# Optimization experiments

Measured on AMD Instinct MI355X. Metric: run time of the kernel, lower is better.

## Reference

```python
import jax, jax.numpy as jnp
import numpy as np


def setup_inputs() -> dict:
    key = jax.random.key(0)
    k1, k2 = jax.random.split(key)
    B, D, H, W, K = 16, 256, 32, 32, 8192
    x = jax.random.normal(k1, (B, D, H, W), dtype=jnp.float32)
    # init_tensor: uniform [0,1), L2-normalized along dim 0 (embedding_dim), * embedding_scale
    e = jax.random.uniform(k2, (D, K), dtype=jnp.float32)
    e_i_ts = e / jnp.linalg.norm(e, axis=0, keepdims=True)
    return {"x": x, "e_i_ts": e_i_ts}


def reference(x, e_i_ts):
    B, D = x.shape[0], x.shape[1]
    spatial = x.shape[2:]
    # permute [B, D, *spatial] -> [B, *spatial, D], flatten tokens
    perm = (0,) + tuple(range(2, x.ndim)) + (1,)
    flat_x = jnp.transpose(x, perm).reshape(-1, D)  # [N, D]
    distances = (
        jnp.sum(flat_x * flat_x, axis=1, keepdims=True)
        - 2.0 * (flat_x @ e_i_ts)
        + jnp.sum(e_i_ts * e_i_ts, axis=0, keepdims=True)
    )
    encoding_indices = jnp.argmin(distances, axis=1)  # [N]
    ind = encoding_indices.reshape((B,) + spatial)  # [B, *spatial]
    # gather codebook columns: e_i_ts.T[ind] -> [B, *spatial, D], back to channel-first
    quantized = jnp.take(e_i_ts.T, ind, axis=0)
    inv_perm = (0, x.ndim - 1) + tuple(range(1, x.ndim - 1))
    quantized_x = jnp.transpose(quantized, inv_perm)  # [B, D, *spatial]
    # straight-through estimator
    quantized_x_d = x + jax.lax.stop_gradient(quantized_x - x)
    return quantized_x_d, quantized_x, ind
```

## Files before the change

### kernel.cpp

```cpp
#include <hip/hip_runtime.h>
#include <hip/hip_bf16.h>
#include <hip/hip_fp16.h>


#define D_   256
#define HW_  1024
#define N_   16384
#define K_   8192
#define NB_  32
#define MARGIN 0.02f

#define OUT1_OFF 4194304
#define IND_OFF  8388608

typedef __attribute__((ext_vector_type(8))) _Float16 f16x8;
typedef __attribute__((ext_vector_type(4))) float f32x4;

__device__ __forceinline__ unsigned long long pack_dk(float dist, int k) {
    unsigned db = __float_as_uint(dist);
    unsigned mono = (db & 0x80000000u) ? ~db : (db | 0x80000000u);
    return ((unsigned long long)mono << 32) | (unsigned)k;
}

__device__ __forceinline__ void async_copy16(const void* g, void* l) {
    __builtin_amdgcn_global_load_lds(
        (const __attribute__((address_space(1))) void*)g,
        (__attribute__((address_space(3))) void*)l, 16, 0, 0);
}

__global__ __launch_bounds__(256)
void cnorm_kernel(const float* __restrict__ E, float* __restrict__ c,
                  int* __restrict__ counters) {
    if (blockIdx.x == 0 && threadIdx.x < 2) counters[threadIdx.x] = 0;
    __shared__ float part[8][32];
    const int tid = threadIdx.x;
    const int cl = tid & 31, q = tid >> 5;
    const int k = blockIdx.x * 32 + cl;
    float s = 0.f;
    #pragma unroll 8
    for (int d = q * 32; d < q * 32 + 32; ++d) {
        float v = E[(size_t)d * K_ + k];
        s = fmaf(v, v, s);
    }
    part[q][cl] = s;
    __syncthreads();
    if (tid < 32) {
        float t0 = (part[0][tid] + part[1][tid]) + (part[2][tid] + part[3][tid]);
        float t1 = (part[4][tid] + part[5][tid]) + (part[6][tid] + part[7][tid]);
        c[blockIdx.x * 32 + tid] = t0 + t1;
    }
}

__global__ __launch_bounds__(256)
void prep_x(const float* __restrict__ x, ushort* __restrict__ xf) {
    __shared__ float t[32][33];
    const int s0 = blockIdx.x * 32, d0 = blockIdx.y * 32, b = blockIdx.z;
    const int tid = threadIdx.x;
    #pragma unroll
    for (int j = 0; j < 4; ++j) {
        int i = tid + 256 * j; int dd = i >> 5, ss = i & 31;
        t[dd][ss] = x[(size_t)b * 262144 + (size_t)(d0 + dd) * 1024 + s0 + ss];
    }
    __syncthreads();
    #pragma unroll
    for (int j = 0; j < 4; ++j) {
        int i = tid + 256 * j; int ss = i >> 5, dd = i & 31;
        _Float16 h = (_Float16)t[dd][ss];
        size_t o = (size_t)(b * 1024 + s0 + ss) * D_ + d0 + dd;
        xf[o] = *(ushort*)&h;
    }
}

__global__ __launch_bounds__(256)
void prep_e(const float* __restrict__ E, ushort* __restrict__ ef) {
    __shared__ float t[32][33];
    const int k0 = blockIdx.x * 32, d0 = blockIdx.y * 32;
    const int tid = threadIdx.x;
    #pragma unroll
    for (int j = 0; j < 4; ++j) {
        int i = tid + 256 * j; int dd = i >> 5, kk = i & 31;
        t[dd][kk] = E[(size_t)(d0 + dd) * K_ + k0 + kk];
    }
    __syncthreads();
    #pragma unroll
    for (int j = 0; j < 4; ++j) {
        int i = tid + 256 * j; int kk = i >> 5, dd = i & 31;
        _Float16 h = (_Float16)t[dd][kk];
        ef[(size_t)(k0 + kk) * D_ + d0 + dd] = *(ushort*)&h;
    }
}

__global__ __launch_bounds__(256, 3)
void mfma_kernel(const ushort* __restrict__ xf,
                 const ushort* __restrict__ ef,
                 const float* __restrict__ c,
                 float* __restrict__ pd1, int* __restrict__ pi1, float* __restrict__ pd2) {
    __shared__ __align__(16) ushort Ah[2][2048];
    __shared__ __align__(16) ushort Bb[2][8192];
    __shared__ float redm1[320], redm2[320];
    __shared__ int   redi1[320];

    const int tid = threadIdx.x;
    const int bid = blockIdx.x;
    const int xcd = bid & 7, rr = bid >> 3;
    const int nb = rr >> 5, mb = xcd * 32 + (rr & 31);
    const int n0 = mb * 64, k0 = nb * 256;
    const int lane = tid & 63, w = tid >> 6;
    const int l15 = lane & 15, lq = lane >> 4;

    size_t aoff;
    {
        int slot = w * 64 + lane;
        int t = slot >> 2, cp = slot & 3;
        int cs = cp ^ ((t >> 1) & 3);
        aoff = (size_t)(n0 + t) * D_ + cs * 8;
    }
    const int adst = w * 512;
    size_t boff[4]; int bdst[4];
    #pragma unroll
    for (int g = 0; g < 4; ++g) {
        int slot = (w * 4 + g) * 64 + lane;
        int t = slot >> 2, cp = slot & 3;
        int cs = cp ^ ((t >> 1) & 3);
        boff[g] = (size_t)(k0 + t) * D_ + cs * 8;
        bdst[g] = (w * 4 + g) * 512;
    }
    int aro[4], bro[4];
    #pragma unroll
    for (int mt = 0; mt < 4; ++mt) {
        int R = mt * 16 + l15;
        aro[mt] = R * 32 + ((lq ^ ((R >> 1) & 3)) * 8);
    }
    #pragma unroll
    for (int nt = 0; nt < 4; ++nt) {
        int R = w * 64 + nt * 16 + l15;
        bro[nt] = R * 32 + ((lq ^ ((R >> 1) & 3)) * 8);
    }

    f32x4 acc[4][4];
    #pragma unroll
    for (int mt = 0; mt < 4; ++mt)
        #pragma unroll
        for (int nt = 0; nt < 4; ++nt) acc[mt][nt] = (f32x4){0.f, 0.f, 0.f, 0.f};

    async_copy16(xf + aoff, &Ah[0][adst]);
    #pragma unroll
    for (int g = 0; g < 4; ++g)
        async_copy16(ef + boff[g], &Bb[0][bdst[g]]);
    __syncthreads();

    #pragma unroll
    for (int db = 0; db < 8; ++db) {
        const int cur = db & 1;
        const int d0 = db * 32;
        if (db < 7) {
            const int dn = d0 + 32;
            async_copy16(xf + aoff + dn, &Ah[cur ^ 1][adst]);
            #pragma unroll
            for (int g = 0; g < 4; ++g)
                async_copy16(ef + boff[g] + dn, &Bb[cur ^ 1][bdst[g]]);
        }
        f16x8 a[4], b[4];
        #pragma unroll
        for (int mt = 0; mt < 4; ++mt)
            a[mt] = *(const f16x8*)&Ah[cur][aro[mt]];
        #pragma unroll
        for (int nt = 0; nt < 4; ++nt)
            b[nt] = *(const f16x8*)&Bb[cur][bro[nt]];
        #pragma unroll
        for (int nt = 0; nt < 4; ++nt)
            #pragma unroll
            for (int mt = 0; mt < 4; ++mt)
                acc[mt][nt] = __builtin_amdgcn_mfma_f32_16x16x32_f16(a[mt], b[nt], acc[mt][nt], 0, 0, 0);
        __syncthreads();
    }

    float cv[4];
    #pragma unroll
    for (int nt = 0; nt < 4; ++nt) cv[nt] = c[k0 + w * 64 + nt * 16 + l15];

    float m1[16], m2[16]; int i1[16];
    #pragma unroll
    for (int mt = 0; mt < 4; ++mt)
        #pragma unroll
        for (int r = 0; r < 4; ++r) {
            int p = mt * 4 + r;
            float a = 3.4e38f, b2 = 3.4e38f; int ai = -1;
            #pragma unroll
            for (int nt = 0; nt < 4; ++nt) {
                float d = fmaf(-2.f, acc[mt][nt][r], cv[nt]);
                int k = k0 + w * 64 + nt * 16 + l15;
                if (d < a) { b2 = a; a = d; ai = k; } else if (d < b2) b2 = d;
            }
            m1[p] = a; i1[p] = ai; m2[p] = b2;
        }
    #pragma unroll
    for (int s = 1; s < 16; s <<= 1) {
        #pragma unroll
        for (int p = 0; p < 16; ++p) {
            float n1 = __shfl_xor(m1[p], s);
            int   ni = __shfl_xor(i1[p], s);
            float n2 = __shfl_xor(m2[p], s);
            if (n1 < m1[p]) { m2[p] = fminf(m1[p], n2); m1[p] = n1; i1[p] = ni; }
            else            { m2[p] = fminf(m2[p], n1); }
        }
    }
    if (l15 == 0) {
        #pragma unroll
        for (int mt = 0; mt < 4; ++mt)
            #pragma unroll
            for (int r = 0; r < 4; ++r) {
                int p = mt * 4 + r;
                int t = mt * 16 + lq * 4 + r;
                redm1[t * 5 + w] = m1[p]; redi1[t * 5 + w] = i1[p]; redm2[t * 5 + w] = m2[p];
            }
    }
    __syncthreads();
    if (tid < 64) {
        float a = redm1[tid * 5], b2 = redm2[tid * 5]; int ai = redi1[tid * 5];
        #pragma unroll
        for (int q = 1; q < 4; ++q) {
            float n1 = redm1[tid * 5 + q], n2 = redm2[tid * 5 + q]; int ni = redi1[tid * 5 + q];
            if (n1 < a) { b2 = fminf(a, n2); a = n1; ai = ni; }
            else        { b2 = fminf(b2, n1); }
        }
        size_t o = (size_t)nb * N_ + n0 + tid;
        pd1[o] = a; pi1[o] = ai; pd2[o] = b2;
    }
}

__global__ __launch_bounds__(256)
void merge_flag(const float* __restrict__ pd1, const int* __restrict__ pi1,
                const float* __restrict__ pd2,
                int* __restrict__ idx, int* __restrict__ counters,
                unsigned long long* __restrict__ key,
                unsigned int* __restrict__ pairs, unsigned int* __restrict__ scans) {
    int n = blockIdx.x * 256 + threadIdx.x;
    float a = 3.4e38f, b2 = 3.4e38f; int ai = -1;
    for (int nb = 0; nb < NB_; ++nb) {
        float n1 = pd1[(size_t)nb * N_ + n];
        int   ni = pi1[(size_t)nb * N_ + n];
        float n2 = pd2[(size_t)nb * N_ + n];
        if (n1 < a) { b2 = fminf(a, n2); a = n1; ai = ni; }
        else        { b2 = fminf(b2, n1); }
    }
    if (b2 - a < MARGIN) {
        const float W = a + MARGIN;
        key[n] = ~0ULL;
        idx[n] = 0x80000000 | ai;
        for (int nb = 0; nb < NB_; ++nb) {
            if (pd2[(size_t)nb * N_ + n] <= W) {
                int q = atomicAdd(&counters[1], 1);
                scans[q] = ((unsigned)n << 5) | (unsigned)nb;
            } else if (pd1[(size_t)nb * N_ + n] <= W) {
                int q = atomicAdd(&counters[0], 1);
                pairs[q] = ((unsigned)n << 13) | (unsigned)pi1[(size_t)nb * N_ + n];
            }
        }
    } else {
        idx[n] = ai;
    }
}

__global__ __launch_bounds__(256)
void recheck(const float* __restrict__ x, const float* __restrict__ E,
             const float* __restrict__ c, const unsigned int* __restrict__ pairs,
             const unsigned int* __restrict__ scans, const int* __restrict__ counters,
             unsigned long long* __restrict__ key) {
    if (blockIdx.x < 128) {
        int items = counters[0] * 4;
        for (int it = blockIdx.x * 256 + threadIdx.x; it < items; it += 128 * 256) {
            int p = it >> 2, q = it & 3;
            unsigned v = pairs[p];
            int n = v >> 13, k = v & 8191;
            int b = n >> 10, s = n & 1023;
            const float* xb = x + (size_t)b * 262144 + s;
            const float* eb = E + k;
            float acc = 0.f;
            const int d0 = q * 64;
            #pragma unroll 8
            for (int d = d0; d < d0 + 64; ++d)
                acc = fmaf(xb[(size_t)d * HW_], eb[(size_t)d * K_], acc);
            float o1 = __shfl_xor(acc, 1); float s2 = acc + o1;
            float o2 = __shfl_xor(s2, 2);  float tot = s2 + o2;
            if (q == 0) atomicMin(key + n, pack_dk(fmaf(-2.f, tot, c[k]), k));
        }
    } else {
        int cnt = counters[1];
        for (int t = blockIdx.x - 128; t < cnt; t += 256) {
            unsigned v = scans[t];
            int n = v >> 5, nb = v & 31;
            int k = nb * 256 + threadIdx.x;
            int b = n >> 10, s = n & 1023;
            const float* xb = x + (size_t)b * 262144 + s;
            float acc = 0.f;
            #pragma unroll 4
            for (int d = 0; d < D_; ++d)
                acc = fmaf(xb[(size_t)d * HW_], E[(size_t)d * K_ + k], acc);
            float dist = fmaf(-2.f, acc, c[k]);
            atomicMin(key + n, pack_dk(dist, k));
        }
    }
}

__global__ __launch_bounds__(256)
void write_kernel(const float* __restrict__ x, const float* __restrict__ E,
                  const int* __restrict__ idx, const unsigned long long* __restrict__ key,
                  float* __restrict__ out) {
    __shared__ int kst[64];
    const int n0 = blockIdx.x * 64;
    const int b = n0 >> 10, s0 = n0 & 1023;
    const int tid = threadIdx.x;
    if (tid < 64) {
        int v = idx[n0 + tid];
        int k = (v < 0) ? (int)(key[n0 + tid] & 8191ULL) : v;
        kst[tid] = k;
        out[IND_OFF + n0 + tid] = (float)k;
    }
    __syncthreads();
    const int g = tid & 15;
    const int d0 = tid >> 4;
    const int ka = kst[g * 4], kb2 = kst[g * 4 + 1], kc = kst[g * 4 + 2], kd = kst[g * 4 + 3];
    const float* xb = x + (size_t)b * 262144 + s0 + g * 4;
    float* o0 = out + (size_t)b * 262144 + s0 + g * 4;
    float* o1 = o0 + OUT1_OFF;
    for (int d = d0; d < D_; d += 16) {
        const float* er = E + (size_t)d * K_;
        float4 xv = *(const float4*)(xb + (size_t)d * HW_);
        float4 q;
        q.x = er[ka]; q.y = er[kb2]; q.z = er[kc]; q.w = er[kd];
        float4 r;
        r.x = xv.x + (q.x - xv.x); r.y = xv.y + (q.y - xv.y);
        r.z = xv.z + (q.z - xv.z); r.w = xv.w + (q.w - xv.w);
        *(float4*)(o0 + (size_t)d * HW_) = r;
        *(float4*)(o1 + (size_t)d * HW_) = q;
    }
}

extern "C" void kernel_launch(void* const* d_in, const int* in_sizes, int n_in,
                              void* d_out, int out_size, void* d_ws, size_t ws_size,
                              hipStream_t stream) {
    const float* x = (const float*)d_in[0];
    const float* E = (const float*)d_in[1];
    float* out = (float*)d_out;

    char* p = (char*)d_ws;
    ushort* xf = (ushort*)p;                 p += (size_t)N_ * D_ * 2;
    ushort* ef = (ushort*)p;                 p += (size_t)K_ * D_ * 2;
    float*  c  = (float*)p;                  p += (size_t)K_ * 4;
    float*  pd1 = (float*)p;                 p += (size_t)NB_ * N_ * 4;
    int*    pi1 = (int*)p;                   p += (size_t)NB_ * N_ * 4;
    float*  pd2 = (float*)p;                 p += (size_t)NB_ * N_ * 4;
    int*    idx = (int*)p;                   p += (size_t)N_ * 4;
    unsigned long long* key = (unsigned long long*)p; p += (size_t)N_ * 8;
    unsigned int* pairs = (unsigned int*)p;  p += (size_t)524288 * 4;
    unsigned int* scans = (unsigned int*)p;  p += (size_t)524288 * 4;
    int*    counters = (int*)p;              p += 256;

    cnorm_kernel<<<K_ / 32, 256, 0, stream>>>(E, c, counters);
    prep_x<<<dim3(32, 8, 16), 256, 0, stream>>>(x, xf);
    prep_e<<<dim3(256, 8), 256, 0, stream>>>(E, ef);
    mfma_kernel<<<8192, 256, 0, stream>>>(xf, ef, c, pd1, pi1, pd2);
    merge_flag<<<N_ / 256, 256, 0, stream>>>(pd1, pi1, pd2, idx, counters, key, pairs, scans);
    recheck<<<384, 256, 0, stream>>>(x, E, c, pairs, scans, counters, key);
    write_kernel<<<N_ / 64, 256, 0, stream>>>(x, E, idx, key, out);
}
```

Baseline: 359.3 us.

## Load MFMA operands directly from global, pack argmin keys, split write kernel

The MFMA kernel drops its LDS double buffering and async global-to-LDS copies and reads f16 fragments straight from global memory into registers, removing the per-step barriers and freeing LDS for occupancy. The top-2 tracking now packs a quantized distance and local code index into one 32-bit unsigned key, which halves the shuffle and shared-memory traffic during the reduction. The cost is that distances are quantized to a 1/32768 grid inside a fixed range, so close ties or out-of-range values rely on the later margin recheck. The write kernel is also split across four D-bands to launch more blocks.

Result: slower. 431.1 us (+20.0%).

```diff
diff --git a/kernel.cpp b/kernel.cpp
--- a/kernel.cpp
+++ b/kernel.cpp
@@ -20,12 +20,6 @@
     unsigned db = __float_as_uint(dist);
     unsigned mono = (db & 0x80000000u) ? ~db : (db | 0x80000000u);
     return ((unsigned long long)mono << 32) | (unsigned)k;
-}
-
-__device__ __forceinline__ void async_copy16(const void* g, void* l) {
-    __builtin_amdgcn_global_load_lds(
-        (const __attribute__((address_space(1))) void*)g,
-        (__attribute__((address_space(3))) void*)l, 16, 0, 0);
 }
 
 __global__ __launch_bounds__(256)
@@ -95,10 +89,7 @@
                  const ushort* __restrict__ ef,
                  const float* __restrict__ c,
                  float* __restrict__ pd1, int* __restrict__ pi1, float* __restrict__ pd2) {
-    __shared__ __align__(16) ushort Ah[2][2048];
-    __shared__ __align__(16) ushort Bb[2][8192];
-    __shared__ float redm1[320], redm2[320];
-    __shared__ int   redi1[320];
+    __shared__ unsigned red1[320], red2[320];
 
     const int tid = threadIdx.x;
     const int bid = blockIdx.x;
@@ -108,34 +99,13 @@
     const int lane = tid & 63, w = tid >> 6;
     const int l15 = lane & 15, lq = lane >> 4;
 
-    size_t aoff;
-    {
-        int slot = w * 64 + lane;
-        int t = slot >> 2, cp = slot & 3;
-        int cs = cp ^ ((t >> 1) & 3);
-        aoff = (size_t)(n0 + t) * D_ + cs * 8;
-    }
-    const int adst = w * 512;
-    size_t boff[4]; int bdst[4];
-    #pragma unroll
-    for (int g = 0; g < 4; ++g) {
-        int slot = (w * 4 + g) * 64 + lane;
-        int t = slot >> 2, cp = slot & 3;
-        int cs = cp ^ ((t >> 1) & 3);
-        boff[g] = (size_t)(k0 + t) * D_ + cs * 8;
-        bdst[g] = (w * 4 + g) * 512;
-    }
-    int aro[4], bro[4];
-    #pragma unroll
-    for (int mt = 0; mt < 4; ++mt) {
-        int R = mt * 16 + l15;
-        aro[mt] = R * 32 + ((lq ^ ((R >> 1) & 3)) * 8);
-    }
-    #pragma unroll
-    for (int nt = 0; nt < 4; ++nt) {
-        int R = w * 64 + nt * 16 + l15;
-        bro[nt] = R * 32 + ((lq ^ ((R >> 1) & 3)) * 8);
-    }
+    const ushort* ap[4]; const ushort* bp[4];
+    #pragma unroll
+    for (int mt = 0; mt < 4; ++mt)
+        ap[mt] = xf + (size_t)(n0 + mt * 16 + l15) * D_ + lq * 8;
+    #pragma unroll
+    for (int nt = 0; nt < 4; ++nt)
+        bp[nt] = ef + (size_t)(k0 + w * 64 + nt * 16 + l15) * D_ + lq * 8;
 
     f32x4 acc[4][4];
     #pragma unroll
@@ -143,66 +113,53 @@
         #pragma unroll
         for (int nt = 0; nt < 4; ++nt) acc[mt][nt] = (f32x4){0.f, 0.f, 0.f, 0.f};
 
-    async_copy16(xf + aoff, &Ah[0][adst]);
-    #pragma unroll
-    for (int g = 0; g < 4; ++g)
-        async_copy16(ef + boff[g], &Bb[0][bdst[g]]);
-    __syncthreads();
-
     #pragma unroll
     for (int db = 0; db < 8; ++db) {
-        const int cur = db & 1;
         const int d0 = db * 32;
-        if (db < 7) {
-            const int dn = d0 + 32;
-            async_copy16(xf + aoff + dn, &Ah[cur ^ 1][adst]);
-            #pragma unroll
-            for (int g = 0; g < 4; ++g)
-                async_copy16(ef + boff[g] + dn, &Bb[cur ^ 1][bdst[g]]);
-        }
         f16x8 a[4], b[4];
         #pragma unroll
-        for (int mt = 0; mt < 4; ++mt)
-            a[mt] = *(const f16x8*)&Ah[cur][aro[mt]];
-        #pragma unroll
-        for (int nt = 0; nt < 4; ++nt)
-            b[nt] = *(const f16x8*)&Bb[cur][bro[nt]];
+        for (int mt = 0; mt < 4; ++mt) a[mt] = *(const f16x8*)(ap[mt] + d0);
+        #pragma unroll
+        for (int nt = 0; nt < 4; ++nt) b[nt] = *(const f16x8*)(bp[nt] + d0);
         #pragma unroll
         for (int nt = 0; nt < 4; ++nt)
             #pragma unroll
             for (int mt = 0; mt < 4; ++mt)
                 acc[mt][nt] = __builtin_amdgcn_mfma_f32_16x16x32_f16(a[mt], b[nt], acc[mt][nt], 0, 0, 0);
-        __syncthreads();
     }
 
     float cv[4];
     #pragma unroll
     for (int nt = 0; nt < 4; ++nt) cv[nt] = c[k0 + w * 64 + nt * 16 + l15];
 
-    float m1[16], m2[16]; int i1[16];
+    unsigned m1[16], m2[16];
     #pragma unroll
     for (int mt = 0; mt < 4; ++mt)
         #pragma unroll
         for (int r = 0; r < 4; ++r) {
             int p = mt * 4 + r;
-            float a = 3.4e38f, b2 = 3.4e38f; int ai = -1;
+            unsigned b1 = 0xFFFFFFFFu, b2v = 0xFFFFFFFFu;
             #pragma unroll
             for (int nt = 0; nt < 4; ++nt) {
-                float d = fmaf(-2.f, acc[mt][nt][r], cv[nt]);
-                int k = k0 + w * 64 + nt * 16 + l15;
-                if (d < a) { b2 = a; a = d; ai = k; } else if (d < b2) b2 = d;
+                float dist = fmaf(-2.f, acc[mt][nt][r], cv[nt]);
+                unsigned u = (unsigned)fmaf(dist, 32768.f, 4194304.f);
+                unsigned key = (u << 8) | (unsigned)(w * 64 + nt * 16 + l15);
+                unsigned t = key > b1 ? key : b1;
+                b1 = key < b1 ? key : b1;
+                b2v = t < b2v ? t : b2v;
             }
-            m1[p] = a; i1[p] = ai; m2[p] = b2;
+            m1[p] = b1; m2[p] = b2v;
         }
     #pragma unroll
     for (int s = 1; s < 16; s <<= 1) {
         #pragma unroll
         for (int p = 0; p < 16; ++p) {
-            float n1 = __shfl_xor(m1[p], s);
-            int   ni = __shfl_xor(i1[p], s);
-            float n2 = __shfl_xor(m2[p], s);
-            if (n1 < m1[p]) { m2[p] = fminf(m1[p], n2); m1[p] = n1; i1[p] = ni; }
-            else            { m2[p] = fminf(m2[p], n1); }
+            unsigned n1 = (unsigned)__shfl_xor((int)m1[p], s);
+            unsigned n2 = (unsigned)__shfl_xor((int)m2[p], s);
+            unsigned t = m1[p] > n1 ? m1[p] : n1;
+            m1[p] = m1[p] < n1 ? m1[p] : n1;
+            unsigned mn = n2 < t ? n2 : t;
+            m2[p] = m2[p] < mn ? m2[p] : mn;
         }
     }
     if (l15 == 0) {
@@ -212,20 +169,24 @@
             for (int r = 0; r < 4; ++r) {
                 int p = mt * 4 + r;
                 int t = mt * 16 + lq * 4 + r;
-                redm1[t * 5 + w] = m1[p]; redi1[t * 5 + w] = i1[p]; redm2[t * 5 + w] = m2[p];
+                red1[t * 5 + w] = m1[p]; red2[t * 5 + w] = m2[p];
             }
     }
     __syncthreads();
     if (tid < 64) {
-        float a = redm1[tid * 5], b2 = redm2[tid * 5]; int ai = redi1[tid * 5];
+        unsigned a1 = red1[tid * 5], a2v = red2[tid * 5];
         #pragma unroll
         for (int q = 1; q < 4; ++q) {
-            float n1 = redm1[tid * 5 + q], n2 = redm2[tid * 5 + q]; int ni = redi1[tid * 5 + q];
-            if (n1 < a) { b2 = fminf(a, n2); a = n1; ai = ni; }
-            else        { b2 = fminf(b2, n1); }
+            unsigned n1 = red1[tid * 5 + q], n2 = red2[tid * 5 + q];
+            unsigned t = a1 > n1 ? a1 : n1;
+            a1 = a1 < n1 ? a1 : n1;
+            unsigned mn = n2 < t ? n2 : t;
+            a2v = a2v < mn ? a2v : mn;
         }
         size_t o = (size_t)nb * N_ + n0 + tid;
-        pd1[o] = a; pi1[o] = ai; pd2[o] = b2;
+        pd1[o] = (float)(a1 >> 8) * (1.f / 32768.f) - 128.f;
+        pi1[o] = k0 + (int)(a1 & 255u);
+        pd2[o] = (float)(a2v >> 8) * (1.f / 32768.f) - 128.f;
     }
 }
 
@@ -315,16 +276,17 @@
         int v = idx[n0 + tid];
         int k = (v < 0) ? (int)(key[n0 + tid] & 8191ULL) : v;
         kst[tid] = k;
-        out[IND_OFF + n0 + tid] = (float)k;
+        if (blockIdx.y == 0) out[IND_OFF + n0 + tid] = (float)k;
     }
     __syncthreads();
     const int g = tid & 15;
     const int d0 = tid >> 4;
+    const int dband = blockIdx.y * 64;
     const int ka = kst[g * 4], kb2 = kst[g * 4 + 1], kc = kst[g * 4 + 2], kd = kst[g * 4 + 3];
     const float* xb = x + (size_t)b * 262144 + s0 + g * 4;
     float* o0 = out + (size_t)b * 262144 + s0 + g * 4;
     float* o1 = o0 + OUT1_OFF;
-    for (int d = d0; d < D_; d += 16) {
+    for (int d = dband + d0; d < dband + 64; d += 16) {
         const float* er = E + (size_t)d * K_;
         float4 xv = *(const float4*)(xb + (size_t)d * HW_);
         float4 q;
@@ -363,5 +325,5 @@
     mfma_kernel<<<8192, 256, 0, stream>>>(xf, ef, c, pd1, pi1, pd2);
     merge_flag<<<N_ / 256, 256, 0, stream>>>(pd1, pi1, pd2, idx, counters, key, pairs, scans);
     recheck<<<384, 256, 0, stream>>>(x, E, c, pairs, scans, counters, key);
-    write_kernel<<<N_ / 64, 256, 0, stream>>>(x, E, idx, key, out);
-}
+    write_kernel<<<dim3(256, 4), 256, 0, stream>>>(x, E, idx, key, out);
+}
```
